# Performance work log

Hardware: AMD Instinct MI355X
Metric: run time of the kernel (lower is better)

Reference implementation:

```python
import jax, jax.numpy as jnp
import numpy as np
from jax import lax

M_BLOCKS = 4
D = 768
N = 8
L = 2040  # divisible by 1,2,3,4 so every block is full, matching the floor-based slicing


def setup_inputs() -> dict:
    key = jax.random.key(0)
    ks = jax.random.split(key, 7)
    X = jax.random.normal(ks[0], (N, L, D), dtype=jnp.float32)
    # char_mixer: Conv1d(d, d, kernel_size=3, padding='same')
    conv_w = jax.random.normal(ks[1], (D, D, 3), dtype=jnp.float32) * (1.0 / np.sqrt(3 * D))
    conv_b = jax.random.normal(ks[2], (D,), dtype=jnp.float32) * 0.01
    # F_R: Linear(d, 1)
    wr = jax.random.normal(ks[3], (D, 1), dtype=jnp.float32) * (1.0 / np.sqrt(D))
    br = jax.random.normal(ks[4], (1,), dtype=jnp.float32) * 0.01
    # F_D: Linear(d, d)
    wd = jax.random.normal(ks[5], (D, D), dtype=jnp.float32) * (1.0 / np.sqrt(D))
    bd = jax.random.normal(ks[6], (D,), dtype=jnp.float32) * 0.01
    return {"X": X, "conv_w": conv_w, "conv_b": conv_b, "wr": wr, "br": br, "wd": wd, "bd": bd}


def reference(X, conv_w, conv_b, wr, br, wd, bd):
    n, l, d = X.shape
    # char mixer: Conv1d over sequence (NCH layout)
    x = lax.conv_general_dilated(
        X.transpose(0, 2, 1), conv_w, window_strides=(1,), padding='SAME',
        dimension_numbers=('NCH', 'OIH', 'NCH'))
    x = (x + conv_b[None, :, None]).transpose(0, 2, 1)  # (N, L, d)

    # multi-scale block-pooled candidates X_B: (N, L, M, d)
    cands = []
    for b in range(1, M_BLOCKS + 1):  # small fixed loop over block sizes
        xb = x.reshape(n, l // b, b, d).mean(axis=2)       # mean-pool F over each block
        cands.append(jnp.repeat(xb, b, axis=1))            # broadcast block mean to positions
    XB = jnp.stack(cands, axis=2)

    # route scores F_R: Linear(d,1); softmax over trailing size-1 dim (faithful to source)
    P = jax.nn.softmax(XB @ wr + br, axis=-1)              # (N, L, M, 1)

    # calibration: softmax(P P^T) P
    P = P.reshape(n, l, M_BLOCKS)
    A = jax.nn.softmax(jnp.einsum('nlm,nkm->nlk', P, P), axis=-1)  # (N, L, L)
    P = jnp.einsum('nlk,nkm->nlm', A, P)                   # (N, L, M)

    # blend candidates and project with F_D
    X_hat = jnp.einsum('nlm,nlmd->nld', P, XB)             # (N, L, d)
    return X_hat @ wd + bd
```

## Files before the change

### kernel.cpp

```cpp
#include <hip/hip_runtime.h>

#define N_B    8
#define L_SEQ  2040
#define D_DIM  768
#define KDIM   2304
#define M_ROWS 16320
#define LPAD   2042

typedef __bf16 bf16x8 __attribute__((ext_vector_type(8)));
typedef float  f32x4  __attribute__((ext_vector_type(4)));

__device__ __forceinline__ unsigned short f2bf_u(float f) {
  union { float f; unsigned u; } v; v.f = f;
  unsigned u = v.u;
  return (unsigned short)((u + 0x7FFFu + ((u >> 16) & 1u)) >> 16);
}

__device__ __forceinline__ void async16(const unsigned short* g, const unsigned char* l) {
  __builtin_amdgcn_global_load_lds(
      (const __attribute__((address_space(1))) void*)g,
      (__attribute__((address_space(3))) void*)l, 16, 0, 0);
}

__global__ void k_pad(const float* __restrict__ X, unsigned short* __restrict__ Xpad) {
  size_t idx = ((size_t)blockIdx.x * 256 + threadIdx.x) * 4;
  const size_t per_n = (size_t)LPAD * D_DIM;
  int n = (int)(idx / per_n);
  size_t rem = idx - (size_t)n * per_n;
  int lp = (int)(rem / D_DIM);
  int d  = (int)(rem - (size_t)lp * D_DIM);
  ushort4 o;
  if (lp == 0 || lp == LPAD - 1) {
    o.x = 0; o.y = 0; o.z = 0; o.w = 0;
  } else {
    const float4 f = *(const float4*)&X[((size_t)n * L_SEQ + (lp - 1)) * D_DIM + d];
    o.x = f2bf_u(f.x); o.y = f2bf_u(f.y); o.z = f2bf_u(f.z); o.w = f2bf_u(f.w);
  }
  *(ushort4*)&Xpad[idx] = o;
}

__global__ void k_tr2(const float* __restrict__ wd, unsigned short* __restrict__ wdT,
                      const float* __restrict__ cw, unsigned short* __restrict__ cwT) {
  __shared__ float tile[32][33];
  const int z = blockIdx.z;
  const float* in = z ? cw : wd;
  unsigned short* out = z ? cwT : wdT;
  const int R = 768, C = z ? 2304 : 768;
  if (!z && blockIdx.x >= 24) return;
  int tx = threadIdx.x, ty = threadIdx.y;
  int c0 = blockIdx.x * 32;
  int r0 = blockIdx.y * 32;
  for (int i = ty; i < 32; i += 8) {
    int r = r0 + i, c = c0 + tx;
    tile[i][tx] = (r < R && c < C) ? in[(size_t)r * C + c] : 0.f;
  }
  __syncthreads();
  for (int i = ty; i < 32; i += 8) {
    int oc = c0 + i;
    int orr = r0 + tx;
    if (oc < C && orr < R) out[(size_t)oc * R + orr] = f2bf_u(tile[tx][i]);
  }
}

__global__ __launch_bounds__(256) void k_w2b(
    const unsigned short* __restrict__ wdT, const unsigned short* __restrict__ cwT,
    unsigned short* __restrict__ Bblk,
    const float* __restrict__ conv_b, const float* __restrict__ wd,
    const float* __restrict__ bd, float* __restrict__ bias2) {
  __shared__ unsigned short sA[128 * 32];
  __shared__ unsigned short sB[128 * 32];
  __shared__ float red[256];
  const int bid = blockIdx.x;
  const int t = threadIdx.x;

  if (bid >= 108) {
    const int b2 = bid - 108;
    const int o = b2 * 64 + (t & 63);
    const int sl = t >> 6;
    float acc = 0.f;
    for (int dm = sl * 192; dm < sl * 192 + 192; ++dm)
      acc += conv_b[dm] * wd[(size_t)dm * D_DIM + o];
    red[t] = acc;
    __syncthreads();
    if (t < 64)
      bias2[o] = 4.f * (red[t] + red[t + 64] + red[t + 128] + red[t + 192]) + bd[o];
    return;
  }

  const int bm = bid / 18, bn = bid - bm * 18;
  const int lane = t & 63, w = t >> 6;
  const int wr = w >> 1, wc = w & 1;
  const int lr = lane & 15, lg = lane >> 4;

  const int c0 = t, c1 = t + 256;
  const unsigned short* aB0 = wdT + (size_t)(bm * 128 + (c0 >> 2)) * 768 + (c0 & 3) * 8;
  const unsigned short* aB1 = wdT + (size_t)(bm * 128 + (c1 >> 2)) * 768 + (c1 & 3) * 8;
  const unsigned short* bB0 = cwT + (size_t)(bn * 128 + (c0 >> 2)) * 768 + (c0 & 3) * 8;
  const unsigned short* bB1 = cwT + (size_t)(bn * 128 + (c1 >> 2)) * 768 + (c1 & 3) * 8;

  f32x4 acc[4][4] = {};
  int aOff[4], bOff[4];
#pragma unroll
  for (int i = 0; i < 4; ++i) {
    aOff[i] = (wr * 64 + i * 16 + lr) * 4 + lg;
    bOff[i] = (wc * 64 + i * 16 + lr) * 4 + lg;
  }
  const bf16x8* At = (const bf16x8*)sA;
  const bf16x8* Bt = (const bf16x8*)sB;

  for (int kt = 0; kt < 24; ++kt) {
    const int ko = kt * 32;
    __syncthreads();
    async16(aB0 + ko, (const unsigned char*)&sA[c0 * 8]);
    async16(aB1 + ko, (const unsigned char*)&sA[c1 * 8]);
    async16(bB0 + ko, (const unsigned char*)&sB[c0 * 8]);
    async16(bB1 + ko, (const unsigned char*)&sB[c1 * 8]);
    __syncthreads();
    bf16x8 av[4], bv[4];
#pragma unroll
    for (int i = 0; i < 4; ++i) { av[i] = At[aOff[i]]; bv[i] = Bt[bOff[i]]; }
#pragma unroll
    for (int mi = 0; mi < 4; ++mi)
#pragma unroll
      for (int ni = 0; ni < 4; ++ni)
        acc[mi][ni] = __builtin_amdgcn_mfma_f32_16x16x32_bf16(av[mi], bv[ni], acc[mi][ni], 0, 0, 0);
  }

#pragma unroll
  for (int ni = 0; ni < 4; ++ni) {
    const int jp = bn * 128 + wc * 64 + ni * 16 + lr;
    const int di = jp / 3;
    const int kk = jp - di * 3;
    const int j = kk * 768 + di;
    const int kt2 = j >> 6, rem = j & 63;
    const int kh = rem >> 5, o = (rem >> 3) & 3, e = rem & 7;
    const size_t jbase = (size_t)kt2 * 16384 + kh * 8192 + o * 128 + e;
#pragma unroll
    for (int mi = 0; mi < 4; ++mi) {
      const int row0 = bm * 128 + wr * 64 + mi * 16 + lg * 4;
      f32x4 v = acc[mi][ni];
#pragma unroll
      for (int i = 0; i < 4; ++i) {
        const int dd = row0 + i;
        const int p = dd >> 8, cl = dd & 255, blk = cl >> 4, r = cl & 15;
        Bblk[(size_t)p * 589824 + jbase + blk * 512 + r * 8] = f2bf_u(v[i]);
      }
    }
  }
}

__global__ __launch_bounds__(512, 2) void k_conv192(
    const unsigned short* __restrict__ Xpad, const unsigned short* __restrict__ Bblk,
    const float* __restrict__ bias2, float* __restrict__ Y) {
  __shared__ unsigned char lds[114688];

  const int tid = threadIdx.x;
  const int lane = tid & 63;
  const int wid = tid >> 6;
  const int wr = wid >> 2, wc = wid & 3;

  const int bid = blockIdx.x;
  const int xcd = bid & 7, idx = bid >> 3;
  const int swz = (xcd < 7 ? xcd * 32 : 224 + (xcd - 7) * 31) + idx;
  const int bm = swz / 3, bn = swz - bm * 3;

  const unsigned short *aS0, *aS1, *aS2;
  {
#define ACHUNK(rr, dst) { \
    int c = tid + (rr) * 512; \
    int kh = c / 768, q = c - kh * 768; \
    int li = q & 63; \
    int rl = (q >> 6) * 16 + (li & 15); \
    int m = bm * 192 + rl; \
    int n = m / L_SEQ, l = m - n * L_SEQ; \
    dst = Xpad + (size_t)(n * LPAD + l) * D_DIM + kh * 32 + (li >> 4) * 8; }
    ACHUNK(0, aS0) ACHUNK(1, aS1) ACHUNK(2, aS2)
#undef ACHUNK
  }
  const unsigned short* bS = Bblk + (size_t)bn * 589824 + tid * 8;
  const int dA0 = tid * 16, dA1 = dA0 + 8192, dA2 = dA0 + 16384;
  const int dB0 = 24576 + tid * 16, dB1 = dB0 + 8192, dB2 = dB0 + 16384, dB3 = dB0 + 24576;

  const int aRd0 = wr * 6144 + lane * 16;
  const int bRd0 = 24576 + wc * 4096 + lane * 16;

  f32x4 acc[6][4] = {};
  bf16x8 avP[6], bvP[4], avQ[6], bvQ[4];

#define STG(src, koff, dst) async16((src) + (koff), lds + nbb + (dst))
#define LD_BANK(bA, bB, kh) \
    _Pragma("unroll") \
    for (int mi = 0; mi < 6; ++mi) \
      bA[mi] = *(const bf16x8*)(lds + cb + aRd0 + (kh) * 12288 + mi * 1024); \
    _Pragma("unroll") \
    for (int ni = 0; ni < 4; ++ni) \
      bB[ni] = *(const bf16x8*)(lds + cb + bRd0 + (kh) * 16384 + (ni) * 1024);
#define MF24(bA, bB) \
    __builtin_amdgcn_s_setprio(1); \
    _Pragma("unroll") \
    for (int mi = 0; mi < 6; ++mi) \
      _Pragma("unroll") \
      for (int ni = 0; ni < 4; ++ni) \
        acc[mi][ni] = __builtin_amdgcn_mfma_f32_16x16x32_bf16(bA[mi], bB[ni], acc[mi][ni], 0, 0, 0); \
    __builtin_amdgcn_s_setprio(0);

  {
    const int nbb = 0;
    STG(aS0, 0, dA0); STG(aS1, 0, dA1); STG(aS2, 0, dA2);
    STG(bS, 0, dB0);  STG(bS, 4096, dB1); STG(bS, 8192, dB2); STG(bS, 12288, dB3);
  }
  __syncthreads();

  for (int t = 0; t < 36; ++t) {
    const int cb = (t & 1) * 57344;
    const int nbb = cb ^ 57344;
    const bool st = (t < 35);
    const int aoff = (t + 1) * 64;
    const size_t boff = (size_t)(t + 1) * 16384;

    LD_BANK(avP, bvP, 0);
    if (st) { STG(aS0, aoff, dA0); STG(aS1, aoff, dA1); STG(aS2, aoff, dA2); }
    LD_BANK(avQ, bvQ, 1);
    if (st) {
      STG(bS, boff, dB0); STG(bS, boff + 4096, dB1);
      STG(bS, boff + 8192, dB2); STG(bS, boff + 12288, dB3);
    }
    MF24(avP, bvP);
    MF24(avQ, bvQ);
    __syncthreads();
  }

  const int lr = lane & 15, lg = lane >> 4;
  const f32x4 bias = *(const f32x4*)&bias2[bn * 256 + lane * 4];
#pragma unroll
  for (int p = 0; p < 2; ++p) {
    if (p) __syncthreads();
    if (wr == p) {
#pragma unroll
      for (int mi = 0; mi < 6; ++mi)
#pragma unroll
        for (int ni = 0; ni < 4; ++ni)
#pragma unroll
          for (int i = 0; i < 4; ++i)
            *(float*)(lds + ((mi * 16 + lg * 4 + i) * 256 + (wc * 64 + ni * 16 + lr)) * 4) =
                acc[mi][ni][i];
    }
    __syncthreads();
    f32x4 y[12];
#pragma unroll
    for (int i = 0; i < 12; ++i)
      y[i] = *(const f32x4*)(lds + ((wid * 12 + i) * 256 + lane * 4) * 4);
    f32x4 m2[6], m3[4], m4[3];
#pragma unroll
    for (int j = 0; j < 6; ++j) m2[j] = (y[2 * j] + y[2 * j + 1]) * 0.5f;
#pragma unroll
    for (int j = 0; j < 4; ++j) m3[j] = (y[3 * j] + y[3 * j + 1] + y[3 * j + 2]) * (1.f / 3.f);
#pragma unroll
    for (int j = 0; j < 3; ++j) m4[j] = (y[4 * j] + y[4 * j + 1] + y[4 * j + 2] + y[4 * j + 3]) * 0.25f;
    const int grow0 = bm * 192 + p * 96 + wid * 12;
#pragma unroll
    for (int i = 0; i < 12; ++i) {
      f32x4 o = y[i] + m2[i >> 1] + m3[i / 3] + m4[i >> 2] + bias;
      *(f32x4*)&Y[(size_t)(grow0 + i) * D_DIM + bn * 256 + lane * 4] = o;
    }
  }
#undef STG
#undef LD_BANK
#undef MF24
}

extern "C" void kernel_launch(void* const* d_in, const int* in_sizes, int n_in,
                              void* d_out, int out_size, void* d_ws, size_t ws_size,
                              hipStream_t stream) {
  const float* X      = (const float*)d_in[0];
  const float* conv_w = (const float*)d_in[1];
  const float* conv_b = (const float*)d_in[2];
  const float* wd     = (const float*)d_in[5];
  const float* bd     = (const float*)d_in[6];
  float* out = (float*)d_out;

  const size_t off_Xpad  = 0;
  const size_t off_wdT   = 25092096;
  const size_t off_cwT   = 26271744;
  const size_t off_Bblk  = 29810688;
  const size_t off_bias2 = 33349632;
  const size_t NEED      = 33352704;
  if (ws_size < NEED) return;

  char* ws = (char*)d_ws;
  unsigned short* Xpad  = (unsigned short*)(ws + off_Xpad);
  unsigned short* wdT   = (unsigned short*)(ws + off_wdT);
  unsigned short* cwT   = (unsigned short*)(ws + off_cwT);
  unsigned short* Bblk  = (unsigned short*)(ws + off_Bblk);
  float*          bias2 = (float*)(ws + off_bias2);

  k_pad<<<12252, 256, 0, stream>>>(X, Xpad);
  k_tr2<<<dim3(72, 24, 2), dim3(32, 8), 0, stream>>>(wd, wdT, conv_w, cwT);
  k_w2b<<<120, 256, 0, stream>>>(wdT, cwT, Bblk, conv_b, wd, bd, bias2);
  k_conv192<<<255, 512, 0, stream>>>(Xpad, Bblk, bias2, out);
}
```

Baseline: 102.4 us.

## Halve GEMM M-tile to 96 rows with 4 waves and single-buffered A

The fused conv/projection GEMM kernel now uses 96-row M tiles with 256 threads (4 waves, each owning all 96 rows by 64 columns) and launches 510 blocks instead of 255. LDS shrinks to about 76KB by single-buffering the A tile while double-buffering B, with explicit waitcnt and sched_barrier ordering so A reloads are issued only after register reads finish. The goal is better CU coverage across the 256 CUs and two blocks per CU. The cost is that each B tile is reused over fewer rows, so more global traffic and staging per output.

```diff
diff --git a/kernel.cpp b/kernel.cpp
--- a/kernel.cpp
+++ b/kernel.cpp
@@ -149,52 +149,51 @@
   }
 }
 
-__global__ __launch_bounds__(512, 2) void k_conv192(
+__global__ __launch_bounds__(256, 2) void k_conv96(
     const unsigned short* __restrict__ Xpad, const unsigned short* __restrict__ Bblk,
     const float* __restrict__ bias2, float* __restrict__ Y) {
-  __shared__ unsigned char lds[114688];
+  __shared__ unsigned char lds[77824];
 
   const int tid = threadIdx.x;
   const int lane = tid & 63;
-  const int wid = tid >> 6;
-  const int wr = wid >> 2, wc = wid & 3;
+  const int wc = tid >> 6;
 
   const int bid = blockIdx.x;
   const int xcd = bid & 7, idx = bid >> 3;
-  const int swz = (xcd < 7 ? xcd * 32 : 224 + (xcd - 7) * 31) + idx;
+  const int swz = (xcd < 6 ? xcd * 64 : 384 + (xcd - 6) * 63) + idx;
   const int bm = swz / 3, bn = swz - bm * 3;
 
   const unsigned short *aS0, *aS1, *aS2;
   {
 #define ACHUNK(rr, dst) { \
-    int c = tid + (rr) * 512; \
-    int kh = c / 768, q = c - kh * 768; \
+    int c = tid + (rr) * 256; \
+    int kh = c / 384, q = c - kh * 384; \
     int li = q & 63; \
     int rl = (q >> 6) * 16 + (li & 15); \
-    int m = bm * 192 + rl; \
+    int m = bm * 96 + rl; \
     int n = m / L_SEQ, l = m - n * L_SEQ; \
     dst = Xpad + (size_t)(n * LPAD + l) * D_DIM + kh * 32 + (li >> 4) * 8; }
     ACHUNK(0, aS0) ACHUNK(1, aS1) ACHUNK(2, aS2)
 #undef ACHUNK
   }
   const unsigned short* bS = Bblk + (size_t)bn * 589824 + tid * 8;
-  const int dA0 = tid * 16, dA1 = dA0 + 8192, dA2 = dA0 + 16384;
-  const int dB0 = 24576 + tid * 16, dB1 = dB0 + 8192, dB2 = dB0 + 16384, dB3 = dB0 + 24576;
-
-  const int aRd0 = wr * 6144 + lane * 16;
-  const int bRd0 = 24576 + wc * 4096 + lane * 16;
+  const int dA = tid * 16;
+  const int dB = tid * 16;
+
+  const int aRd = lane * 16;
+  const int bRd = wc * 4096 + lane * 16;
 
   f32x4 acc[6][4] = {};
-  bf16x8 avP[6], bvP[4], avQ[6], bvQ[4];
-
-#define STG(src, koff, dst) async16((src) + (koff), lds + nbb + (dst))
-#define LD_BANK(bA, bB, kh) \
+  bf16x8 avP[6], avQ[6], bvP[4], bvQ[4];
+
+#define STG_A(koff) do { \
+    async16(aS0 + (koff), lds + dA); \
+    async16(aS1 + (koff), lds + dA + 4096); \
+    async16(aS2 + (koff), lds + dA + 8192); } while (0)
+#define STG_B(nbB, boff) do { \
     _Pragma("unroll") \
-    for (int mi = 0; mi < 6; ++mi) \
-      bA[mi] = *(const bf16x8*)(lds + cb + aRd0 + (kh) * 12288 + mi * 1024); \
-    _Pragma("unroll") \
-    for (int ni = 0; ni < 4; ++ni) \
-      bB[ni] = *(const bf16x8*)(lds + cb + bRd0 + (kh) * 16384 + (ni) * 1024);
+    for (int rr = 0; rr < 8; ++rr) \
+      async16(bS + (boff) + rr * 2048, lds + (nbB) + dB + rr * 4096); } while (0)
 #define MF24(bA, bB) \
     __builtin_amdgcn_s_setprio(1); \
     _Pragma("unroll") \
@@ -204,27 +203,38 @@
         acc[mi][ni] = __builtin_amdgcn_mfma_f32_16x16x32_bf16(bA[mi], bB[ni], acc[mi][ni], 0, 0, 0); \
     __builtin_amdgcn_s_setprio(0);
 
-  {
-    const int nbb = 0;
-    STG(aS0, 0, dA0); STG(aS1, 0, dA1); STG(aS2, 0, dA2);
-    STG(bS, 0, dB0);  STG(bS, 4096, dB1); STG(bS, 8192, dB2); STG(bS, 12288, dB3);
-  }
+  STG_A(0);
+  STG_B(12288, 0);
   __syncthreads();
 
   for (int t = 0; t < 36; ++t) {
-    const int cb = (t & 1) * 57344;
-    const int nbb = cb ^ 57344;
+    const int cbB = 12288 + (t & 1) * 32768;
+    const int nbB = 12288 + ((t & 1) ^ 1) * 32768;
     const bool st = (t < 35);
     const int aoff = (t + 1) * 64;
     const size_t boff = (size_t)(t + 1) * 16384;
 
-    LD_BANK(avP, bvP, 0);
-    if (st) { STG(aS0, aoff, dA0); STG(aS1, aoff, dA1); STG(aS2, aoff, dA2); }
-    LD_BANK(avQ, bvQ, 1);
+#pragma unroll
+    for (int mi = 0; mi < 6; ++mi)
+      avP[mi] = *(const bf16x8*)(lds + aRd + mi * 1024);
+#pragma unroll
+    for (int mi = 0; mi < 6; ++mi)
+      avQ[mi] = *(const bf16x8*)(lds + aRd + 6144 + mi * 1024);
+    __builtin_amdgcn_sched_barrier(0);
+#pragma unroll
+    for (int ni = 0; ni < 4; ++ni)
+      bvP[ni] = *(const bf16x8*)(lds + cbB + bRd + ni * 1024);
+#pragma unroll
+    for (int ni = 0; ni < 4; ++ni)
+      bvQ[ni] = *(const bf16x8*)(lds + cbB + bRd + 16384 + ni * 1024);
+
     if (st) {
-      STG(bS, boff, dB0); STG(bS, boff + 4096, dB1);
-      STG(bS, boff + 8192, dB2); STG(bS, boff + 12288, dB3);
+      asm volatile("s_waitcnt lgkmcnt(8)" ::: "memory");
+      STG_A(aoff);
+      STG_B(nbB, boff);
     }
+    __builtin_amdgcn_sched_barrier(0);
+
     MF24(avP, bvP);
     MF24(avQ, bvQ);
     __syncthreads();
@@ -235,21 +245,19 @@
 #pragma unroll
   for (int p = 0; p < 2; ++p) {
     if (p) __syncthreads();
-    if (wr == p) {
-#pragma unroll
-      for (int mi = 0; mi < 6; ++mi)
-#pragma unroll
-        for (int ni = 0; ni < 4; ++ni)
-#pragma unroll
-          for (int i = 0; i < 4; ++i)
-            *(float*)(lds + ((mi * 16 + lg * 4 + i) * 256 + (wc * 64 + ni * 16 + lr)) * 4) =
-                acc[mi][ni][i];
-    }
+#pragma unroll
+    for (int mi = 0; mi < 3; ++mi)
+#pragma unroll
+      for (int ni = 0; ni < 4; ++ni)
+#pragma unroll
+        for (int i = 0; i < 4; ++i)
+          *(float*)(lds + ((mi * 16 + lg * 4 + i) * 256 + (wc * 64 + ni * 16 + lr)) * 4) =
+              acc[3 * p + mi][ni][i];
     __syncthreads();
     f32x4 y[12];
 #pragma unroll
     for (int i = 0; i < 12; ++i)
-      y[i] = *(const f32x4*)(lds + ((wid * 12 + i) * 256 + lane * 4) * 4);
+      y[i] = *(const f32x4*)(lds + ((wc * 12 + i) * 256 + lane * 4) * 4);
     f32x4 m2[6], m3[4], m4[3];
 #pragma unroll
     for (int j = 0; j < 6; ++j) m2[j] = (y[2 * j] + y[2 * j + 1]) * 0.5f;
@@ -257,15 +265,15 @@
     for (int j = 0; j < 4; ++j) m3[j] = (y[3 * j] + y[3 * j + 1] + y[3 * j + 2]) * (1.f / 3.f);
 #pragma unroll
     for (int j = 0; j < 3; ++j) m4[j] = (y[4 * j] + y[4 * j + 1] + y[4 * j + 2] + y[4 * j + 3]) * 0.25f;
-    const int grow0 = bm * 192 + p * 96 + wid * 12;
+    const int grow0 = bm * 96 + p * 48 + wc * 12;
 #pragma unroll
     for (int i = 0; i < 12; ++i) {
       f32x4 o = y[i] + m2[i >> 1] + m3[i / 3] + m4[i >> 2] + bias;
       *(f32x4*)&Y[(size_t)(grow0 + i) * D_DIM + bn * 256 + lane * 4] = o;
     }
   }
-#undef STG
-#undef LD_BANK
+#undef STG_A
+#undef STG_B
 #undef MF24
 }
 
@@ -297,5 +305,5 @@
   k_pad<<<12252, 256, 0, stream>>>(X, Xpad);
   k_tr2<<<dim3(72, 24, 2), dim3(32, 8), 0, stream>>>(wd, wdT, conv_w, cwT);
   k_w2b<<<120, 256, 0, stream>>>(wdT, cwT, Bblk, conv_b, wd, bd, bias2);
-  k_conv192<<<255, 512, 0, stream>>>(Xpad, Bblk, bias2, out);
-}
+  k_conv96<<<510, 256, 0, stream>>>(Xpad, Bblk, bias2, out);
+}
```

New measurement: 104.0 us. No clear change (+1.5%).
